# Optimization experiments

Hardware: AMD Instinct MI355X
Metric: run time of the kernel (lower is better)

## Reference

```python
import jax, jax.numpy as jnp
import numpy as np
from jax import lax

EPS = 0.01  # BatchNorm eps from the module

def binarize(x):
    # BinarizeF: >= 0 -> +1, < 0 -> -1
    return jnp.where(x >= 0, 1.0, -1.0).astype(x.dtype)

def bintanh(x):
    # binarize(hardtanh(x)); clip doesn't change sign so forward == sign
    return binarize(jnp.clip(x, -1.0, 1.0))

def bn_nch(x, g, b, m, v):
    # BatchNorm1d eval mode over channel axis of [B, C, L]
    scale = g / jnp.sqrt(v + EPS)
    return (x - m[None, :, None]) * scale[None, :, None] + b[None, :, None]

def bn_nc(x, g, b, m, v):
    scale = g / jnp.sqrt(v + EPS)
    return (x - m[None, :]) * scale[None, :] + b[None, :]

def setup_inputs() -> dict:
    key = jax.random.key(0)
    ks = jax.random.split(key, 32)
    B, CIN, W = 65536, 4, 16
    C, H = 32, 64
    d = {
        'x': jax.random.normal(ks[0], (B, CIN, W), jnp.float32),
        'conv0_w': jax.random.normal(ks[1], (C, CIN, 1), jnp.float32) * 0.1,
        'conv0_b': jax.random.normal(ks[2], (C,), jnp.float32) * 0.01,
        'bn0_g': jax.random.uniform(ks[3], (C,), jnp.float32, 0.5, 1.5),
        'bn0_b': jax.random.normal(ks[4], (C,), jnp.float32) * 0.1,
        'bn0_m': jax.random.normal(ks[5], (C,), jnp.float32) * 0.1,
        'bn0_v': jnp.ones((C,), jnp.float32),
        'convs_w': jax.random.normal(ks[6], (4, C, C, 3), jnp.float32) * 0.1,
        'convs_b': jax.random.normal(ks[7], (4, C), jnp.float32) * 0.01,
        'bns_g': jax.random.uniform(ks[8], (4, C), jnp.float32, 0.5, 1.5),
        'bns_b': jax.random.normal(ks[9], (4, C), jnp.float32) * 0.1,
        'bns_m': jax.random.normal(ks[10], (4, C), jnp.float32) * 0.1,
        'bns_v': jnp.ones((4, C), jnp.float32),
        'fc1_w': jax.random.normal(ks[11], (H, C * W), jnp.float32) * 0.05,
        'fc1_b': jax.random.normal(ks[12], (H,), jnp.float32) * 0.01,
        'bn5_g': jax.random.uniform(ks[13], (H,), jnp.float32, 0.5, 1.5),
        'bn5_b': jax.random.normal(ks[14], (H,), jnp.float32) * 0.1,
        'bn5_m': jax.random.normal(ks[15], (H,), jnp.float32) * 0.1,
        'bn5_v': jnp.ones((H,), jnp.float32),
        'fc2_w': jax.random.normal(ks[16], (H, H), jnp.float32) * 0.1,
        'fc2_b': jax.random.normal(ks[17], (H,), jnp.float32) * 0.01,
        'bn6_g': jax.random.uniform(ks[18], (H,), jnp.float32, 0.5, 1.5),
        'bn6_b': jax.random.normal(ks[19], (H,), jnp.float32) * 0.1,
        'bn6_m': jax.random.normal(ks[20], (H,), jnp.float32) * 0.1,
        'bn6_v': jnp.ones((H,), jnp.float32),
        'fc3_w': jax.random.normal(ks[21], (1, H), jnp.float32) * 0.1,
        'fc3_b': jax.random.normal(ks[22], (1,), jnp.float32) * 0.01,
    }
    return d

def reference(x, conv0_w, conv0_b, bn0_g, bn0_b, bn0_m, bn0_v,
              convs_w, convs_b, bns_g, bns_b, bns_m, bns_v,
              fc1_w, fc1_b, bn5_g, bn5_b, bn5_m, bn5_v,
              fc2_w, fc2_b, bn6_g, bn6_b, bn6_m, bn6_v,
              fc3_w, fc3_b):
    B = x.shape[0]
    x = x.reshape(-1, 4, 16)  # (B, n_inputs, word_size)
    # conv0: kernel_size=1 binarized conv -> pointwise channel mix
    y = jnp.einsum('bci,oc->boi', x, binarize(conv0_w[:, :, 0])) + conv0_b[None, :, None]
    y = bintanh(bn_nch(y, bn0_g, bn0_b, bn0_m, bn0_v))
    shortcut = y
    dn = ('NCH', 'OIH', 'NCH')
    for i in range(convs_w.shape[0]):  # numLayers - 1 = 4 fixed blocks
        z = lax.conv_general_dilated(y, binarize(convs_w[i]), (1,), ((1, 1),),
                                     dimension_numbers=dn)
        z = z + convs_b[i][None, :, None]
        z = bn_nch(z, bns_g[i], bns_b[i], bns_m[i], bns_v[i])
        y = bintanh(z) + shortcut  # residual add to first block output
    f = y.reshape(B, -1)  # (B, 32*16)
    h = bintanh(bn_nc(f @ binarize(fc1_w).T + fc1_b, bn5_g, bn5_b, bn5_m, bn5_v))
    h = bintanh(bn_nc(h @ binarize(fc2_w).T + fc2_b, bn6_g, bn6_b, bn6_m, bn6_v))
    out = jax.nn.sigmoid(h @ binarize(fc3_w).T + fc3_b)  # (B, 1)
    return out
```

## Files before the change

### kernel.cpp

```cpp
#include <hip/hip_runtime.h>
#include <hip/hip_bf16.h>
#include <math.h>

typedef unsigned int uint;

#define WB4   0
#define L1S   512
#define L1T   640
#define W1T   672
#define T5O   1696
#define W2T   1760
#define T6O   1888
#define W3O   1952
#define FB3O  1954
#define TOTW  1955

__device__ __forceinline__ float bnr(float v, float cb, float m, float sc, float b) {
  return __fadd_rn(__fmul_rn(__fsub_rn(__fadd_rn(v, cb), m), sc), b);
}

__device__ __forceinline__ int ibs(int lo, int hi, int dir,
                                   float cb, float m, float sc, float b) {
  int ans = hi + 1;
  while (lo <= hi) {
    int mid = lo + ((hi - lo) >> 1);
    float vf = (float)(dir ? -mid : mid);
    if (bnr(vf, cb, m, sc, b) >= 0.f) { ans = mid; hi = mid - 1; }
    else lo = mid + 1;
  }
  return ans;
}

__device__ __forceinline__ float key2f(uint k) {
  return __uint_as_float((k & 0x80000000u) ? (k ^ 0x80000000u) : ~k);
}

__device__ __forceinline__ float fsearch(int dir, float cb, float m, float sc, float b) {
  uint lo = 0x00800000u;
  uint hi = 0xFF7FFFFFu;
  float fhi = key2f(hi);
  if (!(bnr(dir ? -fhi : fhi, cb, m, sc, b) >= 0.f))
    return __uint_as_float(0x7F800000u);
  while (lo < hi) {
    uint mid = lo + ((hi - lo) >> 1);
    float fm = key2f(mid);
    if (bnr(dir ? -fm : fm, cb, m, sc, b) >= 0.f) hi = mid; else lo = mid + 1;
  }
  return key2f(lo);
}

__global__ void prep_kernel(
    const float* __restrict__ conv0_w, const float* __restrict__ conv0_b,
    const float* __restrict__ bn0_g, const float* __restrict__ bn0_b,
    const float* __restrict__ bn0_m, const float* __restrict__ bn0_v,
    const float* __restrict__ convs_w, const float* __restrict__ convs_b,
    const float* __restrict__ bns_g, const float* __restrict__ bns_b,
    const float* __restrict__ bns_m, const float* __restrict__ bns_v,
    const float* __restrict__ fc1_w, const float* __restrict__ fc1_b,
    const float* __restrict__ bn5_g, const float* __restrict__ bn5_b,
    const float* __restrict__ bn5_m, const float* __restrict__ bn5_v,
    const float* __restrict__ fc2_w, const float* __restrict__ fc2_b,
    const float* __restrict__ bn6_g, const float* __restrict__ bn6_b,
    const float* __restrict__ bn6_m, const float* __restrict__ bn6_v,
    const float* __restrict__ fc3_w, const float* __restrict__ fc3_b,
    uint* __restrict__ ws)
{
  const int t0 = blockIdx.x * blockDim.x + threadIdx.x;
  const int NT = gridDim.x * blockDim.x;
  for (int task = t0; task < 1443; task += NT) {
    if (task < 32) {
      int o = task;
      float sc = bn0_g[o] / sqrtf(bn0_v[o] + 0.01f);
      int dir = sc < 0.f;
      uint fm = dir ? 0x80000000u : 0u;
      uint4 sg;
      sg.x = ((conv0_w[o*4+0] >= 0.f) ? 0u : 0x80000000u) ^ fm;
      sg.y = ((conv0_w[o*4+1] >= 0.f) ? 0u : 0x80000000u) ^ fm;
      sg.z = ((conv0_w[o*4+2] >= 0.f) ? 0u : 0x80000000u) ^ fm;
      sg.w = ((conv0_w[o*4+3] >= 0.f) ? 0u : 0x80000000u) ^ fm;
      ((uint4*)(ws + L1S))[o] = sg;
      ((float*)(ws + L1T))[o] = fsearch(dir, conv0_b[o], bn0_m[o], sc, bn0_b[o]);
    } else if (task < 160) {
      int idx = task - 32, k = idx >> 5, o = idx & 31, ko = k * 32 + o;
      float sc = bns_g[ko] / sqrtf(bns_v[ko] + 0.01f);
      int dir = sc < 0.f;
      uint fm = dir ? 0xFFFFFFFFu : 0u;
      uint wv[3];
      for (int d = 0; d < 3; ++d) {
        uint w = 0;
        for (int c = 0; c < 32; ++c)
          if (convs_w[(ko * 32 + c) * 3 + d] >= 0.f) w |= 1u << c;
        wv[d] = w ^ fm;
      }
      int T = ibs(-384, 384, dir, convs_b[ko], bns_m[ko], sc, bns_b[ko]);
      uint4 pk; pk.x = wv[0]; pk.y = wv[1]; pk.z = wv[2]; pk.w = (uint)T;
      ((uint4*)(ws + WB4))[ko] = pk;
    } else if (task < 1184) {
      int u = task - 160, i = u >> 6, j = u & 63;
      float sc = bn5_g[j] / sqrtf(bn5_v[j] + 0.01f);
      uint fm = (sc < 0.f) ? 0xFFFFFFFFu : 0u;
      uint w = 0;
      for (int c = 0; c < 32; ++c)
        if (fc1_w[j * 512 + c * 16 + i] >= 0.f) w |= 1u << c;
      int slot = j * 16 + ((((i >> 2) ^ ((j >> 3) & 3)) << 2) | (i & 3));
      ws[W1T + slot] = w ^ fm;
    } else if (task < 1248) {
      int j = task - 1184;
      float sc = bn5_g[j] / sqrtf(bn5_v[j] + 0.01f);
      int dir = sc < 0.f;
      ((int*)ws)[T5O + j] = ibs(-1025, 1025, dir, fc1_b[j], bn5_m[j], sc, bn5_b[j]);
    } else if (task < 1376) {
      int u = task - 1248, h = u >> 6, j = u & 63;
      float sc = bn6_g[j] / sqrtf(bn6_v[j] + 0.01f);
      uint fm = (sc < 0.f) ? 0xFFFFFFFFu : 0u;
      uint w = 0;
      for (int c = 0; c < 32; ++c)
        if (fc2_w[j * 64 + h * 32 + c] >= 0.f) w |= 1u << c;
      ws[W2T + h * 64 + j] = w ^ fm;
    } else if (task < 1440) {
      int j = task - 1376;
      float sc = bn6_g[j] / sqrtf(bn6_v[j] + 0.01f);
      int dir = sc < 0.f;
      ((int*)ws)[T6O + j] = ibs(-65, 65, dir, fc2_b[j], bn6_m[j], sc, bn6_b[j]);
    } else if (task < 1442) {
      int h = task - 1440;
      uint w = 0;
      for (int c = 0; c < 32; ++c)
        if (fc3_w[h * 32 + c] >= 0.f) w |= 1u << c;
      ws[W3O + h] = w;
    } else {
      ((float*)ws)[FB3O] = fc3_b[0];
    }
  }
}

#define SWZB(v, g) ((uint)__builtin_amdgcn_ds_swizzle((int)(v), ((g) << 5) | 0x18))

__global__ __launch_bounds__(256, 8) void bnn_kernel(const float* __restrict__ x,
                                                     const uint* __restrict__ ws,
                                                     float* __restrict__ out,
                                                     int B)
{
  __shared__ __align__(16) uint sm[TOTW];
  const int gt = blockIdx.x * 256 + threadIdx.x;
  const int b = gt >> 3;
  const int l = gt & 7;

  uint xu0[4], xu1[4];
  if (b < B) {
    const float2* xp = (const float2*)(x + (size_t)b * 64 + 2 * l);
#pragma unroll
    for (int c = 0; c < 4; ++c) {
      float2 v = xp[c * 8];
      xu0[c] = __float_as_uint(v.x);
      xu1[c] = __float_as_uint(v.y);
    }
  }

  for (int i = threadIdx.x; i < TOTW; i += 256) sm[i] = ws[i];
  __syncthreads();
  if (b >= B) return;

  const bool hasL = (l > 0), hasR = (l < 7);
  const uint mL = hasL ? ~0u : 0u;
  const uint mR = hasR ? ~0u : 0u;

  const uint4* l1s = (const uint4*)(sm + L1S);
  const float* l1t = (const float*)(sm + L1T);
  uint s0v0 = 0, s0v1 = 0;
#pragma unroll
  for (int o = 31; o >= 0; --o) {
    uint4 sg = l1s[o];
    float tf = l1t[o];
    float d0 = __fadd_rn(__fadd_rn(__fadd_rn(
                  __uint_as_float(xu0[0] ^ sg.x),
                  __uint_as_float(xu0[1] ^ sg.y)),
                  __uint_as_float(xu0[2] ^ sg.z)),
                  __uint_as_float(xu0[3] ^ sg.w));
    float d1 = __fadd_rn(__fadd_rn(__fadd_rn(
                  __uint_as_float(xu1[0] ^ sg.x),
                  __uint_as_float(xu1[1] ^ sg.y)),
                  __uint_as_float(xu1[2] ^ sg.z)),
                  __uint_as_float(xu1[3] ^ sg.w));
    s0v0 = s0v0 + s0v0 + (uint)(d0 >= tf);
    s0v1 = s0v1 + s0v1 + (uint)(d1 >= tf);
  }

  const uint s0l = (uint)__shfl_up((int)s0v1, 1);
  const uint s0r = (uint)__shfl_down((int)s0v0, 1);

  uint cur0, cur1;

  {
    const int M0 = hasL ? 96 : 64;
    const int M1 = hasR ? 96 : 64;
    const uint4* wb4 = (const uint4*)(sm + WB4);
    uint n0 = 0, n1 = 0;
#pragma unroll
    for (int o = 31; o >= 0; --o) {
      uint4 w = wb4[o];
      int T = (int)w.w;
      int pc0 = __popc(s0v0 ^ w.y) + __popc((s0l ^ w.x) & mL) + __popc(s0v1 ^ w.z);
      int pc1 = __popc(s0v1 ^ w.y) + __popc(s0v0 ^ w.x) + __popc((s0r ^ w.z) & mR);
      n0 = n0 + n0 + (uint)(M0 - 2 * pc0 >= T);
      n1 = n1 + n1 + (uint)(M1 - 2 * pc1 >= T);
    }
    cur0 = n0; cur1 = n1;
  }

  for (int k = 1; k < 4; ++k) {
    const uint cl = (uint)__shfl_up((int)cur1, 1);
    const uint cr = (uint)__shfl_down((int)cur0, 1);
    const uint e0 = ~(cur0 ^ s0v0);
    const uint e1 = ~(cur1 ^ s0v1);
    const uint el = (~(cl ^ s0l)) & mL;
    const uint er = (~(cr ^ s0r)) & mR;
    const int pe0 = __popc(e0), pe1 = __popc(e1);
    const int P2_0 = 2 * (__popc(el) + pe0 + pe1);
    const int P2_1 = 2 * (pe0 + pe1 + __popc(er));
    const uint4* wb4 = (const uint4*)(sm + WB4) + k * 32;
    uint n0 = 0, n1 = 0;
#pragma unroll
    for (int o = 31; o >= 0; --o) {
      uint4 w = wb4[o];
      int T = (int)w.w;
      int pc0 = __popc((cur0 ^ w.y) & e0) + __popc((cl ^ w.x) & el)
              + __popc((cur1 ^ w.z) & e1);
      int pc1 = __popc((cur1 ^ w.y) & e1) + __popc((cur0 ^ w.x) & e0)
              + __popc((cr ^ w.z) & er);
      n0 = n0 + n0 + (uint)(P2_0 - 4 * pc0 >= T);
      n1 = n1 + n1 + (uint)(P2_1 - 4 * pc1 >= T);
    }
    cur0 = n0; cur1 = n1;
  }

  uint curF[16], eF[16];
  int E = 0;
#define GAT(g) { \
    uint cw0 = SWZB(cur0, g), cw1 = SWZB(cur1, g); \
    uint sw0 = SWZB(s0v0, g), sw1 = SWZB(s0v1, g); \
    curF[2*(g)]   = cw0; eF[2*(g)]   = ~(cw0 ^ sw0); \
    curF[2*(g)+1] = cw1; eF[2*(g)+1] = ~(cw1 ^ sw1); \
    E += __popc(eF[2*(g)]) + __popc(eF[2*(g)+1]); }
  GAT(0) GAT(1) GAT(2) GAT(3) GAT(4) GAT(5) GAT(6) GAT(7)
#undef GAT
  const int E2 = 2 * E;

  const int swz = l & 3;
  const uint4* pA = (const uint4*)(sm + W1T + l * 128 + ((0 ^ swz) << 2));
  const uint4* pB = (const uint4*)(sm + W1T + l * 128 + ((1 ^ swz) << 2));
  const uint4* pC = (const uint4*)(sm + W1T + l * 128 + ((2 ^ swz) << 2));
  const uint4* pD = (const uint4*)(sm + W1T + l * 128 + ((3 ^ swz) << 2));
  const int jb = l * 8;
  uint hbits = 0;
#pragma unroll
  for (int jj = 7; jj >= 0; --jj) {
    uint4 wA = pA[jj * 4];
    uint4 wB = pB[jj * 4];
    uint4 wC = pC[jj * 4];
    uint4 wD = pD[jj * 4];
    int pc = 0;
    pc += __popc((curF[0]  ^ wA.x) & eF[0]);
    pc += __popc((curF[1]  ^ wA.y) & eF[1]);
    pc += __popc((curF[2]  ^ wA.z) & eF[2]);
    pc += __popc((curF[3]  ^ wA.w) & eF[3]);
    pc += __popc((curF[4]  ^ wB.x) & eF[4]);
    pc += __popc((curF[5]  ^ wB.y) & eF[5]);
    pc += __popc((curF[6]  ^ wB.z) & eF[6]);
    pc += __popc((curF[7]  ^ wB.w) & eF[7]);
    pc += __popc((curF[8]  ^ wC.x) & eF[8]);
    pc += __popc((curF[9]  ^ wC.y) & eF[9]);
    pc += __popc((curF[10] ^ wC.z) & eF[10]);
    pc += __popc((curF[11] ^ wC.w) & eF[11]);
    pc += __popc((curF[12] ^ wD.x) & eF[12]);
    pc += __popc((curF[13] ^ wD.y) & eF[13]);
    pc += __popc((curF[14] ^ wD.z) & eF[14]);
    pc += __popc((curF[15] ^ wD.w) & eF[15]);
    hbits = hbits + hbits + (uint)(E2 - 4 * pc >= (int)sm[T5O + jb + jj]);
  }
  uint hh = hbits << ((l & 3) * 8);
  uint h0 = (l < 4) ? hh : 0u;
  uint h1 = (l < 4) ? 0u : hh;
  h0 |= (uint)__shfl_xor((int)h0, 1); h0 |= (uint)__shfl_xor((int)h0, 2); h0 |= (uint)__shfl_xor((int)h0, 4);
  h1 |= (uint)__shfl_xor((int)h1, 1); h1 |= (uint)__shfl_xor((int)h1, 2); h1 |= (uint)__shfl_xor((int)h1, 4);

  uint gbits = 0;
#pragma unroll
  for (int jj = 7; jj >= 0; --jj) {
    int pc = __popc(h0 ^ sm[W2T + jb + jj]) + __popc(h1 ^ sm[W2T + 64 + jb + jj]);
    gbits = gbits + gbits + (uint)(64 - 2 * pc >= (int)sm[T6O + jb + jj]);
  }
  uint gg = gbits << ((l & 3) * 8);
  uint g0 = (l < 4) ? gg : 0u;
  uint g1 = (l < 4) ? 0u : gg;
  g0 |= (uint)__shfl_xor((int)g0, 1); g0 |= (uint)__shfl_xor((int)g0, 2); g0 |= (uint)__shfl_xor((int)g0, 4);
  g1 |= (uint)__shfl_xor((int)g1, 1); g1 |= (uint)__shfl_xor((int)g1, 2); g1 |= (uint)__shfl_xor((int)g1, 4);

  if (l == 0) {
    int pc = __popc(g0 ^ sm[W3O]) + __popc(g1 ^ sm[W3O + 1]);
    float z = __fadd_rn((float)(64 - 2 * pc), __uint_as_float(sm[FB3O]));
    out[b] = 1.f / (1.f + expf(-z));
  }
}

extern "C" void kernel_launch(void* const* d_in, const int* in_sizes, int n_in,
                              void* d_out, int out_size, void* d_ws, size_t ws_size,
                              hipStream_t stream) {
  const float* x       = (const float*)d_in[0];
  const float* conv0_w = (const float*)d_in[1];
  const float* conv0_b = (const float*)d_in[2];
  const float* bn0_g   = (const float*)d_in[3];
  const float* bn0_b   = (const float*)d_in[4];
  const float* bn0_m   = (const float*)d_in[5];
  const float* bn0_v   = (const float*)d_in[6];
  const float* convs_w = (const float*)d_in[7];
  const float* convs_b = (const float*)d_in[8];
  const float* bns_g   = (const float*)d_in[9];
  const float* bns_b   = (const float*)d_in[10];
  const float* bns_m   = (const float*)d_in[11];
  const float* bns_v   = (const float*)d_in[12];
  const float* fc1_w   = (const float*)d_in[13];
  const float* fc1_b   = (const float*)d_in[14];
  const float* bn5_g   = (const float*)d_in[15];
  const float* bn5_b   = (const float*)d_in[16];
  const float* bn5_m   = (const float*)d_in[17];
  const float* bn5_v   = (const float*)d_in[18];
  const float* fc2_w   = (const float*)d_in[19];
  const float* fc2_b   = (const float*)d_in[20];
  const float* bn6_g   = (const float*)d_in[21];
  const float* bn6_b   = (const float*)d_in[22];
  const float* bn6_m   = (const float*)d_in[23];
  const float* bn6_v   = (const float*)d_in[24];
  const float* fc3_w   = (const float*)d_in[25];
  const float* fc3_b   = (const float*)d_in[26];
  uint* ws = (uint*)d_ws;

  hipLaunchKernelGGL(prep_kernel, dim3(6), dim3(256), 0, stream,
                     conv0_w, conv0_b, bn0_g, bn0_b, bn0_m, bn0_v,
                     convs_w, convs_b, bns_g, bns_b, bns_m, bns_v,
                     fc1_w, fc1_b, bn5_g, bn5_b, bn5_m, bn5_v,
                     fc2_w, fc2_b, bn6_g, bn6_b, bn6_m, bn6_v,
                     fc3_w, fc3_b, ws);

  const int B = in_sizes[0] / 64;
  const int threads = B * 8;
  hipLaunchKernelGGL(bnn_kernel, dim3((threads + 255) / 256), dim3(256), 0, stream,
                     x, ws, (float*)d_out, B);
}
```

Before: 180.0 us.

## Halve thresholds, use mad_i24 compares, read conv weights from global, shrink LDS

Thresholds for the ternary conv layers and fc1 are pre-halved so that each comparison becomes a single v_mad_i32_i24 (S - 2*pc), removing a shift and subtract per output. Conv and layer-1 weights are now read directly from global memory as uniform loads instead of LDS, so shared memory holds only the fc weights and tables. The layer-1 dot product uses float2 vector adds, and the fc1 enable popcount is reduced by shuffles instead of per-gather popcounts. Launch bounds drop from 8 to 4 waves per SIMD, trading occupancy for registers, and the global weight loads depend on scalar cache behaviour.

```diff
diff --git a/kernel.cpp b/kernel.cpp
--- a/kernel.cpp
+++ b/kernel.cpp
@@ -3,6 +3,7 @@
 #include <math.h>
 
 typedef unsigned int uint;
+typedef float vf2 __attribute__((ext_vector_type(2)));
 
 #define WB4   0
 #define L1S   512
@@ -14,6 +15,13 @@
 #define W3O   1952
 #define FB3O  1954
 #define TOTW  1955
+
+#define ST5   (T5O - W1T)
+#define SW2   (W2T - W1T)
+#define ST6   (T6O - W1T)
+#define SW3   (W3O - W1T)
+#define SFB3  (FB3O - W1T)
+#define SMTOT (TOTW - W1T)
 
 __device__ __forceinline__ float bnr(float v, float cb, float m, float sc, float b) {
   return __fadd_rn(__fmul_rn(__fsub_rn(__fadd_rn(v, cb), m), sc), b);
@@ -93,7 +101,8 @@
         wv[d] = w ^ fm;
       }
       int T = ibs(-384, 384, dir, convs_b[ko], bns_m[ko], sc, bns_b[ko]);
-      uint4 pk; pk.x = wv[0]; pk.y = wv[1]; pk.z = wv[2]; pk.w = (uint)T;
+      int Ts = (k == 0) ? T : ((T + 1) >> 1);
+      uint4 pk; pk.x = wv[0]; pk.y = wv[1]; pk.z = wv[2]; pk.w = (uint)Ts;
       ((uint4*)(ws + WB4))[ko] = pk;
     } else if (task < 1184) {
       int u = task - 160, i = u >> 6, j = u & 63;
@@ -108,7 +117,8 @@
       int j = task - 1184;
       float sc = bn5_g[j] / sqrtf(bn5_v[j] + 0.01f);
       int dir = sc < 0.f;
-      ((int*)ws)[T5O + j] = ibs(-1025, 1025, dir, fc1_b[j], bn5_m[j], sc, bn5_b[j]);
+      int T = ibs(-1025, 1025, dir, fc1_b[j], bn5_m[j], sc, bn5_b[j]);
+      ((int*)ws)[T5O + j] = (T + 1) >> 1;
     } else if (task < 1376) {
       int u = task - 1248, h = u >> 6, j = u & 63;
       float sc = bn6_g[j] / sqrtf(bn6_v[j] + 0.01f);
@@ -134,14 +144,50 @@
   }
 }
 
+__device__ __forceinline__ int madm2(int a, int c) {
+  int d;
+  asm("v_mad_i32_i24 %0, %1, -2, %2" : "=v"(d) : "v"(a), "v"(c));
+  return d;
+}
+
 #define SWZB(v, g) ((uint)__builtin_amdgcn_ds_swizzle((int)(v), ((g) << 5) | 0x18))
 
-__global__ __launch_bounds__(256, 8) void bnn_kernel(const float* __restrict__ x,
+__device__ __forceinline__ void tern_layer(const uint* __restrict__ ws, int koff,
+                                           uint& cur0, uint& cur1,
+                                           uint s0v0, uint s0v1, uint s0l, uint s0r,
+                                           uint mL, uint mR)
+{
+  const uint cl = (uint)__shfl_up((int)cur1, 1);
+  const uint cr = (uint)__shfl_down((int)cur0, 1);
+  const uint e0 = ~(cur0 ^ s0v0);
+  const uint e1 = ~(cur1 ^ s0v1);
+  const uint el = (~(cl ^ s0l)) & mL;
+  const uint er = (~(cr ^ s0r)) & mR;
+  const int pe0 = __popc(e0), pe1 = __popc(e1);
+  const int S0s = __popc(el) + pe0 + pe1;
+  const int S1s = pe0 + pe1 + __popc(er);
+  const uint4* __restrict__ wb = (const uint4*)(ws + WB4) + koff;
+  uint n0 = 0, n1 = 0;
+#pragma unroll
+  for (int o = 31; o >= 0; --o) {
+    uint4 w = wb[o];
+    int Th = (int)w.w;
+    int pc0 = __popc((cur0 ^ w.y) & e0) + (__popc((cl ^ w.x) & el)
+            + __popc((cur1 ^ w.z) & e1));
+    int pc1 = __popc((cur1 ^ w.y) & e1) + (__popc((cur0 ^ w.x) & e0)
+            + __popc((cr ^ w.z) & er));
+    n0 = n0 + n0 + (uint)(madm2(pc0, S0s) >= Th);
+    n1 = n1 + n1 + (uint)(madm2(pc1, S1s) >= Th);
+  }
+  cur0 = n0; cur1 = n1;
+}
+
+__global__ __launch_bounds__(256, 4) void bnn_kernel(const float* __restrict__ x,
                                                      const uint* __restrict__ ws,
                                                      float* __restrict__ out,
                                                      int B)
 {
-  __shared__ __align__(16) uint sm[TOTW];
+  __shared__ __align__(16) uint sm[SMTOT];
   const int gt = blockIdx.x * 256 + threadIdx.x;
   const int b = gt >> 3;
   const int l = gt & 7;
@@ -157,7 +203,7 @@
     }
   }
 
-  for (int i = threadIdx.x; i < TOTW; i += 256) sm[i] = ws[i];
+  for (int i = threadIdx.x; i < SMTOT; i += 256) sm[i] = ws[W1T + i];
   __syncthreads();
   if (b >= B) return;
 
@@ -165,25 +211,20 @@
   const uint mL = hasL ? ~0u : 0u;
   const uint mR = hasR ? ~0u : 0u;
 
-  const uint4* l1s = (const uint4*)(sm + L1S);
-  const float* l1t = (const float*)(sm + L1T);
+  const uint4* __restrict__ l1s = (const uint4*)(ws + L1S);
+  const float* __restrict__ l1t = (const float*)(ws + L1T);
   uint s0v0 = 0, s0v1 = 0;
 #pragma unroll
   for (int o = 31; o >= 0; --o) {
     uint4 sg = l1s[o];
     float tf = l1t[o];
-    float d0 = __fadd_rn(__fadd_rn(__fadd_rn(
-                  __uint_as_float(xu0[0] ^ sg.x),
-                  __uint_as_float(xu0[1] ^ sg.y)),
-                  __uint_as_float(xu0[2] ^ sg.z)),
-                  __uint_as_float(xu0[3] ^ sg.w));
-    float d1 = __fadd_rn(__fadd_rn(__fadd_rn(
-                  __uint_as_float(xu1[0] ^ sg.x),
-                  __uint_as_float(xu1[1] ^ sg.y)),
-                  __uint_as_float(xu1[2] ^ sg.z)),
-                  __uint_as_float(xu1[3] ^ sg.w));
-    s0v0 = s0v0 + s0v0 + (uint)(d0 >= tf);
-    s0v1 = s0v1 + s0v1 + (uint)(d1 >= tf);
+    vf2 v0 = { __uint_as_float(xu0[0] ^ sg.x), __uint_as_float(xu1[0] ^ sg.x) };
+    vf2 v1 = { __uint_as_float(xu0[1] ^ sg.y), __uint_as_float(xu1[1] ^ sg.y) };
+    vf2 v2 = { __uint_as_float(xu0[2] ^ sg.z), __uint_as_float(xu1[2] ^ sg.z) };
+    vf2 v3 = { __uint_as_float(xu0[3] ^ sg.w), __uint_as_float(xu1[3] ^ sg.w) };
+    vf2 d = ((v0 + v1) + v2) + v3;
+    s0v0 = s0v0 + s0v0 + (uint)(d.x >= tf);
+    s0v1 = s0v1 + s0v1 + (uint)(d.y >= tf);
   }
 
   const uint s0l = (uint)__shfl_up((int)s0v1, 1);
@@ -192,65 +233,44 @@
   uint cur0, cur1;
 
   {
-    const int M0 = hasL ? 96 : 64;
-    const int M1 = hasR ? 96 : 64;
-    const uint4* wb4 = (const uint4*)(sm + WB4);
+    const int M0v = hasL ? 96 : 64;
+    const int M1v = hasR ? 96 : 64;
+    const uint4* __restrict__ wb = (const uint4*)(ws + WB4);
     uint n0 = 0, n1 = 0;
 #pragma unroll
     for (int o = 31; o >= 0; --o) {
-      uint4 w = wb4[o];
+      uint4 w = wb[o];
       int T = (int)w.w;
-      int pc0 = __popc(s0v0 ^ w.y) + __popc((s0l ^ w.x) & mL) + __popc(s0v1 ^ w.z);
-      int pc1 = __popc(s0v1 ^ w.y) + __popc(s0v0 ^ w.x) + __popc((s0r ^ w.z) & mR);
-      n0 = n0 + n0 + (uint)(M0 - 2 * pc0 >= T);
-      n1 = n1 + n1 + (uint)(M1 - 2 * pc1 >= T);
+      int pc0 = __popc(s0v0 ^ w.y) + (__popc((s0l ^ w.x) & mL) + __popc(s0v1 ^ w.z));
+      int pc1 = __popc(s0v1 ^ w.y) + (__popc(s0v0 ^ w.x) + __popc((s0r ^ w.z) & mR));
+      n0 = n0 + n0 + (uint)(madm2(pc0, M0v) >= T);
+      n1 = n1 + n1 + (uint)(madm2(pc1, M1v) >= T);
     }
     cur0 = n0; cur1 = n1;
   }
 
-  for (int k = 1; k < 4; ++k) {
-    const uint cl = (uint)__shfl_up((int)cur1, 1);
-    const uint cr = (uint)__shfl_down((int)cur0, 1);
-    const uint e0 = ~(cur0 ^ s0v0);
-    const uint e1 = ~(cur1 ^ s0v1);
-    const uint el = (~(cl ^ s0l)) & mL;
-    const uint er = (~(cr ^ s0r)) & mR;
-    const int pe0 = __popc(e0), pe1 = __popc(e1);
-    const int P2_0 = 2 * (__popc(el) + pe0 + pe1);
-    const int P2_1 = 2 * (pe0 + pe1 + __popc(er));
-    const uint4* wb4 = (const uint4*)(sm + WB4) + k * 32;
-    uint n0 = 0, n1 = 0;
-#pragma unroll
-    for (int o = 31; o >= 0; --o) {
-      uint4 w = wb4[o];
-      int T = (int)w.w;
-      int pc0 = __popc((cur0 ^ w.y) & e0) + __popc((cl ^ w.x) & el)
-              + __popc((cur1 ^ w.z) & e1);
-      int pc1 = __popc((cur1 ^ w.y) & e1) + __popc((cur0 ^ w.x) & e0)
-              + __popc((cr ^ w.z) & er);
-      n0 = n0 + n0 + (uint)(P2_0 - 4 * pc0 >= T);
-      n1 = n1 + n1 + (uint)(P2_1 - 4 * pc1 >= T);
-    }
-    cur0 = n0; cur1 = n1;
-  }
+  tern_layer(ws, 32, cur0, cur1, s0v0, s0v1, s0l, s0r, mL, mR);
+  tern_layer(ws, 64, cur0, cur1, s0v0, s0v1, s0l, s0r, mL, mR);
+  tern_layer(ws, 96, cur0, cur1, s0v0, s0v1, s0l, s0r, mL, mR);
+
+  const uint e0f = ~(cur0 ^ s0v0);
+  const uint e1f = ~(cur1 ^ s0v1);
+  int le = __popc(e0f) + __popc(e1f);
+  le += __shfl_xor(le, 1); le += __shfl_xor(le, 2); le += __shfl_xor(le, 4);
+  const int E = le;
 
   uint curF[16], eF[16];
-  int E = 0;
 #define GAT(g) { \
-    uint cw0 = SWZB(cur0, g), cw1 = SWZB(cur1, g); \
-    uint sw0 = SWZB(s0v0, g), sw1 = SWZB(s0v1, g); \
-    curF[2*(g)]   = cw0; eF[2*(g)]   = ~(cw0 ^ sw0); \
-    curF[2*(g)+1] = cw1; eF[2*(g)+1] = ~(cw1 ^ sw1); \
-    E += __popc(eF[2*(g)]) + __popc(eF[2*(g)+1]); }
+    curF[2*(g)]   = SWZB(cur0, g); curF[2*(g)+1] = SWZB(cur1, g); \
+    eF[2*(g)]     = SWZB(e0f, g);  eF[2*(g)+1]   = SWZB(e1f, g); }
   GAT(0) GAT(1) GAT(2) GAT(3) GAT(4) GAT(5) GAT(6) GAT(7)
 #undef GAT
-  const int E2 = 2 * E;
 
   const int swz = l & 3;
-  const uint4* pA = (const uint4*)(sm + W1T + l * 128 + ((0 ^ swz) << 2));
-  const uint4* pB = (const uint4*)(sm + W1T + l * 128 + ((1 ^ swz) << 2));
-  const uint4* pC = (const uint4*)(sm + W1T + l * 128 + ((2 ^ swz) << 2));
-  const uint4* pD = (const uint4*)(sm + W1T + l * 128 + ((3 ^ swz) << 2));
+  const uint4* pA = (const uint4*)(sm + l * 128 + ((0 ^ swz) << 2));
+  const uint4* pB = (const uint4*)(sm + l * 128 + ((1 ^ swz) << 2));
+  const uint4* pC = (const uint4*)(sm + l * 128 + ((2 ^ swz) << 2));
+  const uint4* pD = (const uint4*)(sm + l * 128 + ((3 ^ swz) << 2));
   const int jb = l * 8;
   uint hbits = 0;
 #pragma unroll
@@ -276,7 +296,7 @@
     pc += __popc((curF[13] ^ wD.y) & eF[13]);
     pc += __popc((curF[14] ^ wD.z) & eF[14]);
     pc += __popc((curF[15] ^ wD.w) & eF[15]);
-    hbits = hbits + hbits + (uint)(E2 - 4 * pc >= (int)sm[T5O + jb + jj]);
+    hbits = hbits + hbits + (uint)(madm2(pc, E) >= (int)sm[ST5 + jb + jj]);
   }
   uint hh = hbits << ((l & 3) * 8);
   uint h0 = (l < 4) ? hh : 0u;
@@ -284,11 +304,12 @@
   h0 |= (uint)__shfl_xor((int)h0, 1); h0 |= (uint)__shfl_xor((int)h0, 2); h0 |= (uint)__shfl_xor((int)h0, 4);
   h1 |= (uint)__shfl_xor((int)h1, 1); h1 |= (uint)__shfl_xor((int)h1, 2); h1 |= (uint)__shfl_xor((int)h1, 4);
 
+  const int c64 = 64;
   uint gbits = 0;
 #pragma unroll
   for (int jj = 7; jj >= 0; --jj) {
-    int pc = __popc(h0 ^ sm[W2T + jb + jj]) + __popc(h1 ^ sm[W2T + 64 + jb + jj]);
-    gbits = gbits + gbits + (uint)(64 - 2 * pc >= (int)sm[T6O + jb + jj]);
+    int pc = __popc(h0 ^ sm[SW2 + jb + jj]) + __popc(h1 ^ sm[SW2 + 64 + jb + jj]);
+    gbits = gbits + gbits + (uint)(madm2(pc, c64) >= (int)sm[ST6 + jb + jj]);
   }
   uint gg = gbits << ((l & 3) * 8);
   uint g0 = (l < 4) ? gg : 0u;
@@ -297,8 +318,8 @@
   g1 |= (uint)__shfl_xor((int)g1, 1); g1 |= (uint)__shfl_xor((int)g1, 2); g1 |= (uint)__shfl_xor((int)g1, 4);
 
   if (l == 0) {
-    int pc = __popc(g0 ^ sm[W3O]) + __popc(g1 ^ sm[W3O + 1]);
-    float z = __fadd_rn((float)(64 - 2 * pc), __uint_as_float(sm[FB3O]));
+    int pc = __popc(g0 ^ sm[SW3]) + __popc(g1 ^ sm[SW3 + 1]);
+    float z = __fadd_rn((float)(64 - 2 * pc), __uint_as_float(sm[SFB3]));
     out[b] = 1.f / (1.f + expf(-z));
   }
 }
```

Result: faster. 172.7 us (median of 2 runs) (-4.1%).
